# Optimization experiments

Hardware: AMD Instinct MI355X
Metric: run time of the kernel (lower is better)

## Reference

```python
import jax, jax.numpy as jnp
import numpy as np

N = 20000
E = 400000
LATENT = 128
HIDDEN = 512
OUT = 64
HEADS = 4
NEG_SLOPE = 0.2


def setup_inputs() -> dict:
    key = jax.random.key(0)
    ks = jax.random.split(key, 12)
    z = jax.random.normal(ks[0], (N, LATENT), dtype=jnp.float32)
    edge_index = jax.random.randint(ks[1], (2, E), 0, N, dtype=jnp.int64)
    h1 = HIDDEN // 2
    # dense1, dense2 (torch Linear: y = x @ W.T + b; store W already transposed)
    W1 = jax.random.normal(ks[2], (LATENT, h1), dtype=jnp.float32) / np.sqrt(LATENT)
    b1 = jnp.zeros((h1,), dtype=jnp.float32)
    W2 = jax.random.normal(ks[3], (h1, HIDDEN), dtype=jnp.float32) / np.sqrt(h1)
    b2 = jnp.zeros((HIDDEN,), dtype=jnp.float32)
    # GATConv params
    Wg = jax.random.normal(ks[4], (HIDDEN, HEADS * OUT), dtype=jnp.float32) / np.sqrt(HIDDEN)
    att_src = jax.random.normal(ks[5], (HEADS, OUT), dtype=jnp.float32) * 0.1
    att_dst = jax.random.normal(ks[6], (HEADS, OUT), dtype=jnp.float32) * 0.1
    bias_g = jnp.zeros((OUT,), dtype=jnp.float32)
    return {"z": z, "W1": W1, "b1": b1, "W2": W2, "b2": b2,
            "Wg": Wg, "att_src": att_src, "att_dst": att_dst, "bias_g": bias_g,
            "edge_index": edge_index}


def _gat(x, Wg, att_src, att_dst, bias_g, src, dst):
    # project: [N, H, D]
    h = (x @ Wg).reshape(N, HEADS, OUT)
    a_src = jnp.einsum('nhd,hd->nh', h, att_src)  # [N, H]
    a_dst = jnp.einsum('nhd,hd->nh', h, att_dst)
    e = a_src[src] + a_dst[dst]                   # [E+N, H]
    e = jax.nn.leaky_relu(e, NEG_SLOPE)
    # segment softmax over destination nodes
    m = jax.ops.segment_max(e, dst, num_segments=N)
    e = jnp.exp(e - m[dst])
    denom = jax.ops.segment_sum(e, dst, num_segments=N)
    w = e / (denom[dst] + 1e-16)                  # [E+N, H]
    msg = h[src] * w[:, :, None]                  # [E+N, H, D]
    out = jax.ops.segment_sum(msg, dst, num_segments=N)  # [N, H, D]
    return out.mean(axis=1) + bias_g              # concat=False -> mean heads


def reference(z, W1, b1, W2, b2, Wg, att_src, att_dst, bias_g, edge_index):
    x = jax.nn.relu(z @ W1 + b1)
    x = jax.nn.relu(x @ W2 + b2)
    # PyG GATConv default add_self_loops=True
    loop = jnp.arange(N, dtype=edge_index.dtype)
    src = jnp.concatenate([edge_index[0], loop])
    dst = jnp.concatenate([edge_index[1], loop])
    return _gat(x, Wg, att_src, att_dst, bias_g, src, dst)
```

## Files before the change

### kernel.cpp

```cpp
#include <hip/hip_runtime.h>
#include <hip/hip_bf16.h>

#define N_NODES 20000
#define MPAD    20096
#define E_EDGES 400000
#define LATENT 128
#define H1 256
#define HIDDEN 512
#define OUT_D 64
#define HEADS 4
#define NEG_SLOPE 0.2f
#define MAX_IN 80


typedef __attribute__((ext_vector_type(8))) __bf16 bf16x8;
typedef __attribute__((ext_vector_type(4))) float f32x4;
typedef __attribute__((ext_vector_type(4))) unsigned short u16x4;
typedef __attribute__((ext_vector_type(8))) unsigned short u16x8;

__device__ __forceinline__ unsigned short f2bf(float f) {
    union { float f; unsigned int u; } v; v.f = f;
    unsigned int r = v.u + 0x7fffu + ((v.u >> 16) & 1u);
    return (unsigned short)(r >> 16);
}
__device__ __forceinline__ float bf2f(unsigned short u) {
    union { unsigned int u; float f; } v; v.u = ((unsigned int)u) << 16;
    return v.f;
}

#define W1_TILES 32
#define W2_TILES 128
#define WG_TILES 128
#define CUR_BLKS ((N_NODES + 255) / 256)
#define PREP_BLKS (W1_TILES + W2_TILES + WG_TILES + CUR_BLKS)
__global__ __launch_bounds__(256)
void prep_kernel(const float* __restrict__ W1, const float* __restrict__ W2,
                 const float* __restrict__ Wg,
                 unsigned short* __restrict__ W1t, unsigned short* __restrict__ W2t,
                 unsigned short* __restrict__ Wgt, int* __restrict__ cur) {
    int b = blockIdx.x;
    if (b >= W1_TILES + W2_TILES + WG_TILES) {
        int t = (b - (W1_TILES + W2_TILES + WG_TILES)) * 256 + threadIdx.x;
        if (t < N_NODES) cur[t] = 0;
        return;
    }
    const float* src; unsigned short* dst; int K, N, k0, n0;
    if (b < W1_TILES) {
        src = W1; dst = W1t; K = LATENT; N = H1;
        k0 = (b >> 3) * 32; n0 = (b & 7) * 32;
    } else if (b < W1_TILES + W2_TILES) {
        int t2 = b - W1_TILES;
        src = W2; dst = W2t; K = H1; N = HIDDEN;
        k0 = (t2 >> 4) * 32; n0 = (t2 & 15) * 32;
    } else {
        int t3 = b - W1_TILES - W2_TILES;
        src = Wg; dst = Wgt; K = HIDDEN; N = HEADS * OUT_D;
        k0 = (t3 >> 3) * 32; n0 = (t3 & 7) * 32;
    }
    __shared__ float tile[32][33];
    const int c = threadIdx.x & 31, r0 = threadIdx.x >> 5;
#pragma unroll
    for (int i = 0; i < 4; i++) {
        int r = r0 + i * 8;
        tile[r][c] = src[(size_t)(k0 + r) * N + n0 + c];
    }
    __syncthreads();
#pragma unroll
    for (int i = 0; i < 4; i++) {
        int r = r0 + i * 8;
        dst[(size_t)(n0 + r) * K + k0 + c] = f2bf(tile[c][r]);
    }
}

#define TM 32
#define ZPITCH 136
#define XPITCH 264
#define X2PITCH 520
#define MLP_BLOCKS (MPAD / TM)
#define SCAT_BLOCKS 140
__global__ __launch_bounds__(256, 4)
void mlp_scatter_kernel(const float* __restrict__ z,
                        const unsigned short* __restrict__ W1t,
                        const unsigned short* __restrict__ W2t,
                        const unsigned short* __restrict__ Wgt,
                        const float* __restrict__ b1, const float* __restrict__ b2,
                        const float* __restrict__ att_src, const float* __restrict__ att_dst,
                        const int* __restrict__ ei, int* __restrict__ cur,
                        unsigned short* __restrict__ adj,
                        unsigned short* __restrict__ hb,
                        float* __restrict__ a_src, float* __restrict__ a_dst) {
    __shared__ unsigned short x2s[TM * X2PITCH];
    __shared__ unsigned short x1s[TM * XPITCH];

    if (blockIdx.x >= MLP_BLOCKS) {
        int t0 = (blockIdx.x - MLP_BLOCKS) * 256 + threadIdx.x;
        for (int t = t0; t < E_EDGES; t += SCAT_BLOCKS * 256) {
            int s = ei[t], d = ei[E_EDGES + t];
            int idx = atomicAdd(&cur[d], 1);
            idx = min(idx, MAX_IN - 1);
            adj[d * MAX_IN + idx] = (unsigned short)s;
        }
        return;
    }

    unsigned short* zbf = x2s;
    const int tid = threadIdx.x;
    const int wave = tid >> 6, lane = tid & 63;
    const int m0 = blockIdx.x * TM;
    const int fr = lane & 15, q = lane >> 4;

#define LDW1(kt, t)      (*(const bf16x8*)(W1t + (size_t)(nb1 + (t) * 16 + fr) * LATENT + (kt) * 32 + q * 8))
#define LDW2H(nh, kt, t) (*(const bf16x8*)(W2t + (size_t)(nb2 + (nh) * 64 + (t) * 16 + fr) * H1 + (kt) * 32 + q * 8))
#define LDW3(kt, t)      (*(const bf16x8*)(Wgt + (size_t)(nb3 + (t) * 16 + fr) * HIDDEN + (kt) * 32 + q * 8))

    const int nb1 = wave * 64;
    const int nb2 = wave * 128;
    const int head = wave;
    const int nb3 = wave * 64;

    bf16x8 w1a[4], w1b[4];
#pragma unroll
    for (int t = 0; t < 4; t++) w1a[t] = LDW1(0, t);

    {
        const int r = tid >> 3, c0 = (tid & 7) * 16;
        const int zrow = min(m0 + r, N_NODES - 1);
        const float* zp = z + (size_t)zrow * LATENT + c0;
#pragma unroll
        for (int i = 0; i < 4; i++) {
            f32x4 v = *(const f32x4*)(zp + i * 4);
            u16x4 p = { f2bf(v[0]), f2bf(v[1]), f2bf(v[2]), f2bf(v[3]) };
            *(u16x4*)(zbf + r * ZPITCH + c0 + i * 4) = p;
        }
    }
    __syncthreads();

    f32x4 acc1[2][4] = {};
#pragma unroll
    for (int kt = 0; kt < 4; kt++) {
        bf16x8* wc = (kt & 1) ? w1b : w1a;
        bf16x8* wn = (kt & 1) ? w1a : w1b;
        if (kt < 3) {
#pragma unroll
            for (int t = 0; t < 4; t++) wn[t] = LDW1(kt + 1, t);
        }
        bf16x8 af[2];
#pragma unroll
        for (int t = 0; t < 2; t++)
            af[t] = *(const bf16x8*)(zbf + (t * 16 + fr) * ZPITCH + kt * 32 + q * 8);
#pragma unroll
        for (int mt = 0; mt < 2; mt++)
#pragma unroll
            for (int nt = 0; nt < 4; nt++)
                acc1[mt][nt] = __builtin_amdgcn_mfma_f32_16x16x32_bf16(
                    wc[nt], af[mt], acc1[mt][nt], 0, 0, 0);
    }

    bf16x8 w2a[4], w2b[4];
#pragma unroll
    for (int t = 0; t < 4; t++) w2a[t] = LDW2H(0, 0, t);

#pragma unroll
    for (int nt = 0; nt < 4; nt++) {
        const int n = nb1 + nt * 16 + q * 4;
        const f32x4 bv = *(const f32x4*)(b1 + n);
#pragma unroll
        for (int mt = 0; mt < 2; mt++) {
            u16x4 p;
#pragma unroll
            for (int r = 0; r < 4; r++) p[r] = f2bf(fmaxf(acc1[mt][nt][r] + bv[r], 0.f));
            *(u16x4*)(x1s + (mt * 16 + fr) * XPITCH + n) = p;
        }
    }
    __syncthreads();

#pragma unroll
    for (int nh = 0; nh < 2; nh++) {
        if (nh == 1) {
#pragma unroll
            for (int t = 0; t < 4; t++) w2a[t] = LDW2H(1, 0, t);
        }
        f32x4 acc2[2][4] = {};
#pragma unroll
        for (int kt = 0; kt < 8; kt++) {
            bf16x8* wc = (kt & 1) ? w2b : w2a;
            bf16x8* wn = (kt & 1) ? w2a : w2b;
            if (kt < 7) {
#pragma unroll
                for (int t = 0; t < 4; t++) wn[t] = LDW2H(nh, kt + 1, t);
            }
            bf16x8 af[2];
#pragma unroll
            for (int t = 0; t < 2; t++)
                af[t] = *(const bf16x8*)(x1s + (t * 16 + fr) * XPITCH + kt * 32 + q * 8);
#pragma unroll
            for (int mt = 0; mt < 2; mt++)
#pragma unroll
                for (int nt = 0; nt < 4; nt++)
                    acc2[mt][nt] = __builtin_amdgcn_mfma_f32_16x16x32_bf16(
                        wc[nt], af[mt], acc2[mt][nt], 0, 0, 0);
        }
#pragma unroll
        for (int nt = 0; nt < 4; nt++) {
            const int n = nb2 + nh * 64 + nt * 16 + q * 4;
            const f32x4 bv = *(const f32x4*)(b2 + n);
#pragma unroll
            for (int mt = 0; mt < 2; mt++) {
                u16x4 p;
#pragma unroll
                for (int r = 0; r < 4; r++) p[r] = f2bf(fmaxf(acc2[mt][nt][r] + bv[r], 0.f));
                *(u16x4*)(x2s + (mt * 16 + fr) * X2PITCH + n) = p;
            }
        }
    }

    bf16x8 w3a[4], w3b[4];
#pragma unroll
    for (int t = 0; t < 4; t++) w3a[t] = LDW3(0, t);
    __syncthreads();

    f32x4 acc3[2][4] = {};
#pragma unroll
    for (int kt = 0; kt < 16; kt++) {
        bf16x8* wc = (kt & 1) ? w3b : w3a;
        bf16x8* wn = (kt & 1) ? w3a : w3b;
        if (kt < 15) {
#pragma unroll
            for (int t = 0; t < 4; t++) wn[t] = LDW3(kt + 1, t);
        }
        bf16x8 af[2];
#pragma unroll
        for (int t = 0; t < 2; t++)
            af[t] = *(const bf16x8*)(x2s + (t * 16 + fr) * X2PITCH + kt * 32 + q * 8);
#pragma unroll
        for (int mt = 0; mt < 2; mt++)
#pragma unroll
            for (int nt = 0; nt < 4; nt++)
                acc3[mt][nt] = __builtin_amdgcn_mfma_f32_16x16x32_bf16(
                    wc[nt], af[mt], acc3[mt][nt], 0, 0, 0);
    }

    {
        f32x4 asv[4], adv[4];
#pragma unroll
        for (int nt = 0; nt < 4; nt++) {
            asv[nt] = *(const f32x4*)(att_src + head * OUT_D + nt * 16 + q * 4);
            adv[nt] = *(const f32x4*)(att_dst + head * OUT_D + nt * 16 + q * 4);
        }
#pragma unroll
        for (int mt = 0; mt < 2; mt++) {
            const int row = m0 + mt * 16 + fr;
            float vs = 0.f, vd = 0.f;
#pragma unroll
            for (int nt = 0; nt < 4; nt++) {
                u16x4 p;
#pragma unroll
                for (int r = 0; r < 4; r++) {
                    float x = acc3[mt][nt][r];
                    p[r] = f2bf(x);
                    vs += x * asv[nt][r];
                    vd += x * adv[nt][r];
                }
                *(u16x4*)(hb + (size_t)row * (HEADS * OUT_D) + head * OUT_D + nt * 16 + q * 4) = p;
            }
            vs += __shfl_xor(vs, 16, 64); vs += __shfl_xor(vs, 32, 64);
            vd += __shfl_xor(vd, 16, 64); vd += __shfl_xor(vd, 32, 64);
            if (q == 0 && row < N_NODES) {
                a_src[row * HEADS + head] = vs;
                a_dst[row * HEADS + head] = vd;
            }
        }
    }
#undef LDW1
#undef LDW2H
#undef LDW3
}

__global__ __launch_bounds__(256)
void fused_gat(const unsigned short* __restrict__ adj, const int* __restrict__ cur,
               const float* __restrict__ a_src, const float* __restrict__ a_dst,
               const unsigned short* __restrict__ hb,
               const float* __restrict__ bias_g, float* __restrict__ out) {
    const int wave = threadIdx.x >> 6, lane = threadIdx.x & 63;
    const int grp = lane >> 5, sl = lane & 31;
    const int d = blockIdx.x * 8 + wave * 2 + grp;
    const int h = sl >> 3, j = sl & 7;
    const int cnt = min(cur[d], MAX_IN);
    const unsigned short* arow = adj + d * MAX_IN;
    const int gbase = grp * 32;

    int myadj = (sl < cnt) ? (int)arow[sl] : 0;

    const float ad = a_dst[d * HEADS + h];
    const unsigned short* hp = hb + h * OUT_D + j * 8;

    float vself = a_src[d * HEADS + h] + ad;
    vself = (vself > 0.f) ? vself : NEG_SLOPE * vself;
    float sm = __expf(fminf(vself, 60.f));
    u16x8 gs = *(const u16x8*)(hp + (size_t)d * (HEADS * OUT_D));
    float acc[8];
#pragma unroll
    for (int r = 0; r < 8; r++) acc[r] = sm * bf2f(gs[r]);

    const int lim = cnt < 32 ? cnt : 32;
    int e = 0;
    for (; e + 7 < lim; e += 8) {
        int sx[8]; float fx[8]; u16x8 gx[8];
#pragma unroll
        for (int u = 0; u < 8; u++) sx[u] = __shfl(myadj, gbase + e + u, 64);
#pragma unroll
        for (int u = 0; u < 8; u++) fx[u] = a_src[sx[u] * HEADS + h];
#pragma unroll
        for (int u = 0; u < 8; u++) gx[u] = *(const u16x8*)(hp + (size_t)sx[u] * (HEADS * OUT_D));
#pragma unroll
        for (int u = 0; u < 8; u++) {
            float v = fx[u] + ad;
            v = (v > 0.f) ? v : NEG_SLOPE * v;
            float w = __expf(fminf(v, 60.f));
            sm += w;
#pragma unroll
            for (int r = 0; r < 8; r++) acc[r] += w * bf2f(gx[u][r]);
        }
    }
    for (; e + 3 < lim; e += 4) {
        int sx[4]; float fx[4]; u16x8 gx[4];
#pragma unroll
        for (int u = 0; u < 4; u++) sx[u] = __shfl(myadj, gbase + e + u, 64);
#pragma unroll
        for (int u = 0; u < 4; u++) fx[u] = a_src[sx[u] * HEADS + h];
#pragma unroll
        for (int u = 0; u < 4; u++) gx[u] = *(const u16x8*)(hp + (size_t)sx[u] * (HEADS * OUT_D));
#pragma unroll
        for (int u = 0; u < 4; u++) {
            float v = fx[u] + ad;
            v = (v > 0.f) ? v : NEG_SLOPE * v;
            float w = __expf(fminf(v, 60.f));
            sm += w;
#pragma unroll
            for (int r = 0; r < 8; r++) acc[r] += w * bf2f(gx[u][r]);
        }
    }
    for (; e < lim; e++) {
        int s = __shfl(myadj, gbase + e, 64);
        float v = a_src[s * HEADS + h] + ad;
        v = (v > 0.f) ? v : NEG_SLOPE * v;
        float w = __expf(fminf(v, 60.f));
        u16x8 g = *(const u16x8*)(hp + (size_t)s * (HEADS * OUT_D));
        sm += w;
#pragma unroll
        for (int r = 0; r < 8; r++) acc[r] += w * bf2f(g[r]);
    }
    for (int e2 = 32; e2 < cnt; e2++) {
        int s = arow[e2];
        float v = a_src[s * HEADS + h] + ad;
        v = (v > 0.f) ? v : NEG_SLOPE * v;
        float w = __expf(fminf(v, 60.f));
        u16x8 g = *(const u16x8*)(hp + (size_t)s * (HEADS * OUT_D));
        sm += w;
#pragma unroll
        for (int r = 0; r < 8; r++) acc[r] += w * bf2f(g[r]);
    }

    const float inv = 1.f / (sm + 1e-16f);
#pragma unroll
    for (int r = 0; r < 8; r++) {
        acc[r] *= inv;
        acc[r] += __shfl_xor(acc[r], 8, 64);
        acc[r] += __shfl_xor(acc[r], 16, 64);
    }
    if (h == 0) {
        const f32x4 bg0 = *(const f32x4*)(bias_g + j * 8);
        const f32x4 bg1 = *(const f32x4*)(bias_g + j * 8 + 4);
        f32x4 o0 = { 0.25f * acc[0] + bg0[0], 0.25f * acc[1] + bg0[1],
                     0.25f * acc[2] + bg0[2], 0.25f * acc[3] + bg0[3] };
        f32x4 o1 = { 0.25f * acc[4] + bg1[0], 0.25f * acc[5] + bg1[1],
                     0.25f * acc[6] + bg1[2], 0.25f * acc[7] + bg1[3] };
        *(f32x4*)(out + (size_t)d * OUT_D + j * 8) = o0;
        *(f32x4*)(out + (size_t)d * OUT_D + j * 8 + 4) = o1;
    }
}

extern "C" void kernel_launch(void* const* d_in, const int* in_sizes, int n_in,
                              void* d_out, int out_size, void* d_ws, size_t ws_size,
                              hipStream_t stream) {
    const float* z       = (const float*)d_in[0];
    const float* W1      = (const float*)d_in[1];
    const float* b1      = (const float*)d_in[2];
    const float* W2      = (const float*)d_in[3];
    const float* b2      = (const float*)d_in[4];
    const float* Wg      = (const float*)d_in[5];
    const float* att_src = (const float*)d_in[6];
    const float* att_dst = (const float*)d_in[7];
    const float* bias_g  = (const float*)d_in[8];
    const int*   ei      = (const int*)d_in[9];
    float* out = (float*)d_out;

    char* ws = (char*)d_ws;
    size_t off = 0;
    auto carve = [&](size_t bytes) { void* p = ws + off; off += (bytes + 255) & ~(size_t)255; return p; };

    unsigned short* W1t = (unsigned short*)carve((size_t)H1 * LATENT * 2);
    unsigned short* W2t = (unsigned short*)carve((size_t)HIDDEN * H1 * 2);
    unsigned short* Wgt = (unsigned short*)carve((size_t)(HEADS * OUT_D) * HIDDEN * 2);
    unsigned short* hb  = (unsigned short*)carve((size_t)MPAD * HEADS * OUT_D * 2);
    float* a_src = (float*)carve((size_t)N_NODES * HEADS * 4);
    float* a_dst = (float*)carve((size_t)N_NODES * HEADS * 4);
    int*   cur   = (int*)carve((size_t)N_NODES * 4);
    unsigned short* adj = (unsigned short*)carve((size_t)MAX_IN * N_NODES * 2);

    prep_kernel<<<PREP_BLKS, 256, 0, stream>>>(W1, W2, Wg, W1t, W2t, Wgt, cur);

    mlp_scatter_kernel<<<MLP_BLOCKS + SCAT_BLOCKS, 256, 0, stream>>>(
        z, W1t, W2t, Wgt, b1, b2, att_src, att_dst, ei, cur, adj, hb, a_src, a_dst);

    fused_gat<<<N_NODES / 8, 256, 0, stream>>>(
        adj, cur, a_src, a_dst, hb, bias_g, out);
}
```

Measured before the change: 160.7 us.

## Split MLP work across eight waves per block with cross-wave attention reduction

Doubles the MLP/scatter block size to 512 threads so each wave computes half as many output columns in each layer. Each head's attention dot products are now split across two waves and combined through shared memory after an extra barrier. The aim is more waves in flight and fewer registers per wave to hide weight-load latency. The cost is an extra synchronisation and the same weights being loaded by more waves per block.

```diff
diff --git a/kernel.cpp b/kernel.cpp
--- a/kernel.cpp
+++ b/kernel.cpp
@@ -78,7 +78,7 @@
 #define X2PITCH 520
 #define MLP_BLOCKS (MPAD / TM)
 #define SCAT_BLOCKS 140
-__global__ __launch_bounds__(256, 4)
+__global__ __launch_bounds__(512, 6)
 void mlp_scatter_kernel(const float* __restrict__ z,
                         const unsigned short* __restrict__ W1t,
                         const unsigned short* __restrict__ W2t,
@@ -93,8 +93,8 @@
     __shared__ unsigned short x1s[TM * XPITCH];
 
     if (blockIdx.x >= MLP_BLOCKS) {
-        int t0 = (blockIdx.x - MLP_BLOCKS) * 256 + threadIdx.x;
-        for (int t = t0; t < E_EDGES; t += SCAT_BLOCKS * 256) {
+        int t0 = (blockIdx.x - MLP_BLOCKS) * 512 + threadIdx.x;
+        for (int t = t0; t < E_EDGES; t += SCAT_BLOCKS * 512) {
             int s = ei[t], d = ei[E_EDGES + t];
             int idx = atomicAdd(&cur[d], 1);
             idx = min(idx, MAX_IN - 1);
@@ -109,25 +109,24 @@
     const int m0 = blockIdx.x * TM;
     const int fr = lane & 15, q = lane >> 4;
 
-#define LDW1(kt, t)      (*(const bf16x8*)(W1t + (size_t)(nb1 + (t) * 16 + fr) * LATENT + (kt) * 32 + q * 8))
-#define LDW2H(nh, kt, t) (*(const bf16x8*)(W2t + (size_t)(nb2 + (nh) * 64 + (t) * 16 + fr) * H1 + (kt) * 32 + q * 8))
-#define LDW3(kt, t)      (*(const bf16x8*)(Wgt + (size_t)(nb3 + (t) * 16 + fr) * HIDDEN + (kt) * 32 + q * 8))
-
-    const int nb1 = wave * 64;
-    const int nb2 = wave * 128;
-    const int head = wave;
-    const int nb3 = wave * 64;
-
-    bf16x8 w1a[4], w1b[4];
-#pragma unroll
-    for (int t = 0; t < 4; t++) w1a[t] = LDW1(0, t);
+#define LDW1(kt, t) (*(const bf16x8*)(W1t + (size_t)(nb1 + (t) * 16 + fr) * LATENT + (kt) * 32 + q * 8))
+#define LDW2(kt, t) (*(const bf16x8*)(W2t + (size_t)(nb2 + (t) * 16 + fr) * H1 + (kt) * 32 + q * 8))
+#define LDW3(kt, t) (*(const bf16x8*)(Wgt + (size_t)(nb3 + (t) * 16 + fr) * HIDDEN + (kt) * 32 + q * 8))
+
+    const int nb1 = wave * 32;
+    const int nb2 = wave * 64;
+    const int nb3 = wave * 32;
+
+    bf16x8 w1a[2], w1b[2];
+#pragma unroll
+    for (int t = 0; t < 2; t++) w1a[t] = LDW1(0, t);
 
     {
-        const int r = tid >> 3, c0 = (tid & 7) * 16;
+        const int r = tid >> 4, c0 = (tid & 15) * 8;
         const int zrow = min(m0 + r, N_NODES - 1);
         const float* zp = z + (size_t)zrow * LATENT + c0;
 #pragma unroll
-        for (int i = 0; i < 4; i++) {
+        for (int i = 0; i < 2; i++) {
             f32x4 v = *(const f32x4*)(zp + i * 4);
             u16x4 p = { f2bf(v[0]), f2bf(v[1]), f2bf(v[2]), f2bf(v[3]) };
             *(u16x4*)(zbf + r * ZPITCH + c0 + i * 4) = p;
@@ -135,14 +134,14 @@
     }
     __syncthreads();
 
-    f32x4 acc1[2][4] = {};
+    f32x4 acc1[2][2] = {};
 #pragma unroll
     for (int kt = 0; kt < 4; kt++) {
         bf16x8* wc = (kt & 1) ? w1b : w1a;
         bf16x8* wn = (kt & 1) ? w1a : w1b;
         if (kt < 3) {
 #pragma unroll
-            for (int t = 0; t < 4; t++) wn[t] = LDW1(kt + 1, t);
+            for (int t = 0; t < 2; t++) wn[t] = LDW1(kt + 1, t);
         }
         bf16x8 af[2];
 #pragma unroll
@@ -151,17 +150,17 @@
 #pragma unroll
         for (int mt = 0; mt < 2; mt++)
 #pragma unroll
-            for (int nt = 0; nt < 4; nt++)
+            for (int nt = 0; nt < 2; nt++)
                 acc1[mt][nt] = __builtin_amdgcn_mfma_f32_16x16x32_bf16(
                     wc[nt], af[mt], acc1[mt][nt], 0, 0, 0);
     }
 
     bf16x8 w2a[4], w2b[4];
 #pragma unroll
-    for (int t = 0; t < 4; t++) w2a[t] = LDW2H(0, 0, t);
-
-#pragma unroll
-    for (int nt = 0; nt < 4; nt++) {
+    for (int t = 0; t < 4; t++) w2a[t] = LDW2(0, t);
+
+#pragma unroll
+    for (int nt = 0; nt < 2; nt++) {
         const int n = nb1 + nt * 16 + q * 4;
         const f32x4 bv = *(const f32x4*)(b1 + n);
 #pragma unroll
@@ -174,59 +173,53 @@
     }
     __syncthreads();
 
-#pragma unroll
-    for (int nh = 0; nh < 2; nh++) {
-        if (nh == 1) {
-#pragma unroll
-            for (int t = 0; t < 4; t++) w2a[t] = LDW2H(1, 0, t);
-        }
-        f32x4 acc2[2][4] = {};
-#pragma unroll
-        for (int kt = 0; kt < 8; kt++) {
-            bf16x8* wc = (kt & 1) ? w2b : w2a;
-            bf16x8* wn = (kt & 1) ? w2a : w2b;
-            if (kt < 7) {
-#pragma unroll
-                for (int t = 0; t < 4; t++) wn[t] = LDW2H(nh, kt + 1, t);
-            }
-            bf16x8 af[2];
-#pragma unroll
-            for (int t = 0; t < 2; t++)
-                af[t] = *(const bf16x8*)(x1s + (t * 16 + fr) * XPITCH + kt * 32 + q * 8);
-#pragma unroll
-            for (int mt = 0; mt < 2; mt++)
-#pragma unroll
-                for (int nt = 0; nt < 4; nt++)
-                    acc2[mt][nt] = __builtin_amdgcn_mfma_f32_16x16x32_bf16(
-                        wc[nt], af[mt], acc2[mt][nt], 0, 0, 0);
-        }
-#pragma unroll
-        for (int nt = 0; nt < 4; nt++) {
-            const int n = nb2 + nh * 64 + nt * 16 + q * 4;
-            const f32x4 bv = *(const f32x4*)(b2 + n);
-#pragma unroll
-            for (int mt = 0; mt < 2; mt++) {
-                u16x4 p;
-#pragma unroll
-                for (int r = 0; r < 4; r++) p[r] = f2bf(fmaxf(acc2[mt][nt][r] + bv[r], 0.f));
-                *(u16x4*)(x2s + (mt * 16 + fr) * X2PITCH + n) = p;
-            }
-        }
-    }
-
-    bf16x8 w3a[4], w3b[4];
-#pragma unroll
-    for (int t = 0; t < 4; t++) w3a[t] = LDW3(0, t);
+    f32x4 acc2[2][4] = {};
+#pragma unroll
+    for (int kt = 0; kt < 8; kt++) {
+        bf16x8* wc = (kt & 1) ? w2b : w2a;
+        bf16x8* wn = (kt & 1) ? w2a : w2b;
+        if (kt < 7) {
+#pragma unroll
+            for (int t = 0; t < 4; t++) wn[t] = LDW2(kt + 1, t);
+        }
+        bf16x8 af[2];
+#pragma unroll
+        for (int t = 0; t < 2; t++)
+            af[t] = *(const bf16x8*)(x1s + (t * 16 + fr) * XPITCH + kt * 32 + q * 8);
+#pragma unroll
+        for (int mt = 0; mt < 2; mt++)
+#pragma unroll
+            for (int nt = 0; nt < 4; nt++)
+                acc2[mt][nt] = __builtin_amdgcn_mfma_f32_16x16x32_bf16(
+                    wc[nt], af[mt], acc2[mt][nt], 0, 0, 0);
+    }
+
+    bf16x8 w3a[2], w3b[2];
+#pragma unroll
+    for (int t = 0; t < 2; t++) w3a[t] = LDW3(0, t);
+
+#pragma unroll
+    for (int nt = 0; nt < 4; nt++) {
+        const int n = nb2 + nt * 16 + q * 4;
+        const f32x4 bv = *(const f32x4*)(b2 + n);
+#pragma unroll
+        for (int mt = 0; mt < 2; mt++) {
+            u16x4 p;
+#pragma unroll
+            for (int r = 0; r < 4; r++) p[r] = f2bf(fmaxf(acc2[mt][nt][r] + bv[r], 0.f));
+            *(u16x4*)(x2s + (mt * 16 + fr) * X2PITCH + n) = p;
+        }
+    }
     __syncthreads();
 
-    f32x4 acc3[2][4] = {};
+    f32x4 acc3[2][2] = {};
 #pragma unroll
     for (int kt = 0; kt < 16; kt++) {
         bf16x8* wc = (kt & 1) ? w3b : w3a;
         bf16x8* wn = (kt & 1) ? w3a : w3b;
         if (kt < 15) {
 #pragma unroll
-            for (int t = 0; t < 4; t++) wn[t] = LDW3(kt + 1, t);
+            for (int t = 0; t < 2; t++) wn[t] = LDW3(kt + 1, t);
         }
         bf16x8 af[2];
 #pragma unroll
@@ -235,24 +228,26 @@
 #pragma unroll
         for (int mt = 0; mt < 2; mt++)
 #pragma unroll
-            for (int nt = 0; nt < 4; nt++)
+            for (int nt = 0; nt < 2; nt++)
                 acc3[mt][nt] = __builtin_amdgcn_mfma_f32_16x16x32_bf16(
                     wc[nt], af[mt], acc3[mt][nt], 0, 0, 0);
     }
 
     {
-        f32x4 asv[4], adv[4];
-#pragma unroll
-        for (int nt = 0; nt < 4; nt++) {
-            asv[nt] = *(const f32x4*)(att_src + head * OUT_D + nt * 16 + q * 4);
-            adv[nt] = *(const f32x4*)(att_dst + head * OUT_D + nt * 16 + q * 4);
-        }
+        const int head = wave >> 1, half = wave & 1;
+        f32x4 asv[2], adv[2];
+#pragma unroll
+        for (int nt = 0; nt < 2; nt++) {
+            asv[nt] = *(const f32x4*)(att_src + head * OUT_D + half * 32 + nt * 16 + q * 4);
+            adv[nt] = *(const f32x4*)(att_dst + head * OUT_D + half * 32 + nt * 16 + q * 4);
+        }
+        float* red = (float*)x1s;
 #pragma unroll
         for (int mt = 0; mt < 2; mt++) {
             const int row = m0 + mt * 16 + fr;
             float vs = 0.f, vd = 0.f;
 #pragma unroll
-            for (int nt = 0; nt < 4; nt++) {
+            for (int nt = 0; nt < 2; nt++) {
                 u16x4 p;
 #pragma unroll
                 for (int r = 0; r < 4; r++) {
@@ -261,18 +256,33 @@
                     vs += x * asv[nt][r];
                     vd += x * adv[nt][r];
                 }
-                *(u16x4*)(hb + (size_t)row * (HEADS * OUT_D) + head * OUT_D + nt * 16 + q * 4) = p;
+                *(u16x4*)(hb + (size_t)row * (HEADS * OUT_D) + head * OUT_D + half * 32
+                          + nt * 16 + q * 4) = p;
             }
             vs += __shfl_xor(vs, 16, 64); vs += __shfl_xor(vs, 32, 64);
             vd += __shfl_xor(vd, 16, 64); vd += __shfl_xor(vd, 32, 64);
-            if (q == 0 && row < N_NODES) {
-                a_src[row * HEADS + head] = vs;
-                a_dst[row * HEADS + head] = vd;
+            if (q == 0) {
+                red[((mt * 16 + fr) * 8 + wave) * 2 + 0] = vs;
+                red[((mt * 16 + fr) * 8 + wave) * 2 + 1] = vd;
             }
         }
+        __syncthreads();
+        if (wave < HEADS) {
+#pragma unroll
+            for (int mt = 0; mt < 2; mt++) {
+                const int row = m0 + mt * 16 + fr;
+                if (q == 0 && row < N_NODES) {
+                    const int ri = (mt * 16 + fr) * 8;
+                    float vs = red[(ri + 2 * wave) * 2 + 0] + red[(ri + 2 * wave + 1) * 2 + 0];
+                    float vd = red[(ri + 2 * wave) * 2 + 1] + red[(ri + 2 * wave + 1) * 2 + 1];
+                    a_src[row * HEADS + wave] = vs;
+                    a_dst[row * HEADS + wave] = vd;
+                }
+            }
+        }
     }
 #undef LDW1
-#undef LDW2H
+#undef LDW2
 #undef LDW3
 }
 
@@ -410,7 +420,7 @@
 
     prep_kernel<<<PREP_BLKS, 256, 0, stream>>>(W1, W2, Wg, W1t, W2t, Wgt, cur);
 
-    mlp_scatter_kernel<<<MLP_BLOCKS + SCAT_BLOCKS, 256, 0, stream>>>(
+    mlp_scatter_kernel<<<MLP_BLOCKS + SCAT_BLOCKS, 512, 0, stream>>>(
         z, W1t, W2t, Wgt, b1, b2, att_src, att_dst, ei, cur, adj, hb, a_src, a_dst);
 
     fused_gat<<<N_NODES / 8, 256, 0, stream>>>(
```

Measured after the change: 161.0 us. About the same (+0.2%).
